# Performance work log

Hardware: AMD Instinct MI355X
Metric: run time of the kernel (lower is better)

The kernel has to match this reference:

```python
import jax, jax.numpy as jnp
import numpy as np

NUM_NODES = 20000
SEQ_LEN = 128
IN_FEATS = 2
HIDDEN = 32
N_TOTAL = NUM_NODES * SEQ_LEN  # flattened graph size
N_EDGES = 2_000_000


def setup_inputs() -> dict:
    key = jax.random.key(0)
    ks = jax.random.split(key, 10)
    x = jax.random.normal(ks[0], (NUM_NODES, SEQ_LEN, IN_FEATS), dtype=jnp.float32)
    edge_index = jax.random.randint(ks[1], (2, N_EDGES), 0, N_TOTAL, dtype=jnp.int64)
    s = 0.1
    gcn_W = jax.random.normal(ks[2], (IN_FEATS, HIDDEN), dtype=jnp.float32) * s
    gcn_b = jnp.zeros((HIDDEN,), dtype=jnp.float32)
    w_ih = jax.random.normal(ks[3], (4 * HIDDEN, HIDDEN), dtype=jnp.float32) * s
    w_hh = jax.random.normal(ks[4], (4 * HIDDEN, HIDDEN), dtype=jnp.float32) * s
    b_ih = jax.random.normal(ks[5], (4 * HIDDEN,), dtype=jnp.float32) * s
    b_hh = jax.random.normal(ks[6], (4 * HIDDEN,), dtype=jnp.float32) * s
    fc_W = jax.random.normal(ks[7], (HIDDEN, 1), dtype=jnp.float32) * s
    fc_b = jnp.zeros((1,), dtype=jnp.float32)
    return {"x": x, "edge_index": edge_index, "gcn_W": gcn_W, "gcn_b": gcn_b,
            "w_ih": w_ih, "w_hh": w_hh, "b_ih": b_ih, "b_hh": b_hh,
            "fc_W": fc_W, "fc_b": fc_b}


def _gcn(x_flat, edge_index, W, b):
    # PyG GCNConv: add self-loops, symmetric normalization, then linear+bias.
    src, dst = edge_index[0], edge_index[1]
    n = x_flat.shape[0]
    # degree at target side, including the self-loop (+1)
    deg = jax.ops.segment_sum(jnp.ones_like(dst, dtype=x_flat.dtype), dst, num_segments=n) + 1.0
    dinv = jax.lax.rsqrt(deg)  # deg >= 1 always (self-loop)
    h = x_flat @ W  # [n, HIDDEN] transform before propagate
    norm = dinv[src] * dinv[dst]  # [E]
    msg = h[src] * norm[:, None]  # gather + per-edge scale
    agg = jax.ops.segment_sum(msg, dst, num_segments=n)
    # self-loop contribution: dinv_i * dinv_i * h_i = h_i / deg_i
    out = agg + h * (1.0 / deg)[:, None]
    return out + b


def _lstm(xs, w_ih, w_hh, b_ih, b_hh):
    # torch LSTM gate order: i, f, g, o. xs: [N, S, H] -> final hidden [N, H]
    n, s, hdim = xs.shape
    xs_t = jnp.swapaxes(xs, 0, 1)  # [S, N, H]
    # precompute input projections once (dense GEMM)
    x_proj = xs_t @ w_ih.T + b_ih + b_hh  # [S, N, 4H]

    def step(carry, xp):
        h, c = carry
        g = xp + h @ w_hh.T  # [N, 4H]
        i, f, gg, o = jnp.split(g, 4, axis=-1)
        c = jax.nn.sigmoid(f) * c + jax.nn.sigmoid(i) * jnp.tanh(gg)
        h = jax.nn.sigmoid(o) * jnp.tanh(c)
        return (h, c), None

    h0 = jnp.zeros((n, hdim), dtype=xs.dtype)
    (hn, _), _ = jax.lax.scan(step, (h0, h0), x_proj)
    return hn


def reference(x, edge_index, gcn_W, gcn_b, w_ih, w_hh, b_ih, b_hh, fc_W, fc_b):
    num_nodes, seq_len, num_feats = x.shape
    x_in = x.reshape(-1, num_feats)  # [N*S, F]
    x_gcn = jax.nn.relu(_gcn(x_in, edge_index, gcn_W, gcn_b))
    x_lstm = x_gcn.reshape(num_nodes, seq_len, -1)
    hn = _lstm(x_lstm, w_ih, w_hh, b_ih, b_hh)
    return hn @ fc_W + fc_b  # [num_nodes, 1]
```

## Files before the change

kernel.cpp:

```cpp
#include <hip/hip_runtime.h>

#define SEQ 128
#define HID 32
#define TPB2 128
#define XS 40

typedef __attribute__((ext_vector_type(8))) short short8;
typedef __attribute__((ext_vector_type(4))) float floatx4;


__global__ void count_kernel(const int* __restrict__ idx, int E, int* __restrict__ cnt) {
    int e = (blockIdx.x * blockDim.x + threadIdx.x) * 4;
    if (((E & 3) == 0) && e + 3 < E) {
        int4 d = *(const int4*)(idx + E + e);
        atomicAdd(&cnt[d.x], 1);
        atomicAdd(&cnt[d.y], 1);
        atomicAdd(&cnt[d.z], 1);
        atomicAdd(&cnt[d.w], 1);
    } else {
        int lim = min(e + 4, E);
        for (int k = e; k < lim; ++k) atomicAdd(&cnt[idx[E + k]], 1);
    }
}

__device__ __forceinline__ unsigned long long pk2(float xx, float yy, float dv) {
    int qx = __float2int_rn(xx * dv * 2097152.0f);
    int qy = __float2int_rn(yy * dv * 2097152.0f);
    return ((unsigned long long)(unsigned)(qx + (1 << 26)) << 32) |
           (unsigned)(qy + (1 << 26));
}

__global__ void scatter_pk_kernel(const int* __restrict__ idx, int E,
                                  const float2* __restrict__ x2,
                                  const int* __restrict__ deg,
                                  unsigned long long* __restrict__ aggP) {
    int e = (blockIdx.x * blockDim.x + threadIdx.x) * 4;
    if (((E & 3) == 0) && e + 3 < E) {
        int4 s = *(const int4*)(idx + e);
        int4 d = *(const int4*)(idx + E + e);
        float2 v0 = x2[s.x];
        float2 v1 = x2[s.y];
        float2 v2 = x2[s.z];
        float2 v3 = x2[s.w];
        float dv0 = rsqrtf((float)deg[s.x] + 1.0f);
        float dv1 = rsqrtf((float)deg[s.y] + 1.0f);
        float dv2 = rsqrtf((float)deg[s.z] + 1.0f);
        float dv3 = rsqrtf((float)deg[s.w] + 1.0f);
        atomicAdd(&aggP[d.x], pk2(v0.x, v0.y, dv0));
        atomicAdd(&aggP[d.y], pk2(v1.x, v1.y, dv1));
        atomicAdd(&aggP[d.z], pk2(v2.x, v2.y, dv2));
        atomicAdd(&aggP[d.w], pk2(v3.x, v3.y, dv3));
    } else {
        int lim = min(e + 4, E);
        for (int k = e; k < lim; ++k) {
            int s = idx[k];
            int d = idx[E + k];
            float2 v = x2[s];
            float dv = rsqrtf((float)deg[s] + 1.0f);
            atomicAdd(&aggP[d], pk2(v.x, v.y, dv));
        }
    }
}


__device__ __forceinline__ float sg(float y) {
    return __builtin_amdgcn_rcpf(1.0f + __builtin_amdgcn_exp2f(-y));
}
__device__ __forceinline__ float tanh_f(float x) {
    return fmaf(__builtin_amdgcn_rcpf(1.0f + __expf(-2.0f * x)), 2.0f, -1.0f);
}
__device__ __forceinline__ void fsplit(float f, short& hi, short& lo) {
    unsigned u = __float_as_uint(f);
    hi = (short)(u >> 16);
    float r = f - __uint_as_float(u & 0xFFFF0000u);
    lo = (short)(__float_as_uint(r) >> 16);
}
__device__ __forceinline__ void fsplit2(float a, float b, unsigned& hi, unsigned& lo) {
    unsigned ta = __float_as_uint(a) & 0xFFFF0000u;
    unsigned tb = __float_as_uint(b) & 0xFFFF0000u;
    float ra = a - __uint_as_float(ta);
    float rb = b - __uint_as_float(tb);
    hi = __builtin_amdgcn_perm(__float_as_uint(b), __float_as_uint(a), 0x07060302u);
    lo = __builtin_amdgcn_perm(__float_as_uint(rb), __float_as_uint(ra), 0x07060302u);
}

__global__ __launch_bounds__(TPB2, 3) void lstm_sw3_kernel(
    const float2* __restrict__ x2,
    const unsigned long long* __restrict__ aggP, const int* __restrict__ deg,
    int N,
    const float* __restrict__ gcn_W, const float* __restrict__ gcn_b,
    const float* __restrict__ w_ih, const float* __restrict__ w_hh,
    const float* __restrict__ b_ih, const float* __restrict__ b_hh,
    const float* __restrict__ fc_W, const float* __restrict__ fc_b,
    float* __restrict__ out) {
    __shared__ float2 ubuf[16][SEQ + 1];
    __shared__ __align__(16) short hhb[2][16][XS];
    __shared__ __align__(16) short hlb[2][16][XS];
    __shared__ __align__(16) short xgh[2][16][XS];
    __shared__ __align__(16) short xgl[2][16][XS];
    __shared__ float fcp[2][16];

    const int tid = threadIdx.x;
    const int t1 = tid >> 6;
    const int lane = tid & 63;
    const int n = lane & 15;
    const int q = lane >> 4;
    const int base = blockIdx.x * 16;

    {
        const float2* xb = x2 + (size_t)base * SEQ;
        const unsigned long long* apb = aggP + (size_t)base * SEQ;
        const int* dgb = deg + (size_t)base * SEQ;
        const int lim = min(16 * SEQ, (N - base) * SEQ);
        for (int i = tid; i < 16 * SEQ; i += TPB2) {
            float2 v = make_float2(0.f, 0.f);
            if (i < lim) {
                int dg = dgb[i];
                float dv = rsqrtf((float)dg + 1.0f);
                float2 xx = xb[i];
                unsigned long long pk = apb[i];
                unsigned bias = (unsigned)dg * 67108864u;
                float ax = (float)((int)((unsigned)(pk >> 32) - bias)) * (1.0f / 2097152.0f);
                float ay = (float)((int)((unsigned)pk - bias)) * (1.0f / 2097152.0f);
                v = make_float2(dv * fmaf(xx.x, dv, ax), dv * fmaf(xx.y, dv, ay));
            }
            ubuf[i >> 7][i & 127] = v;
        }
        if (tid < 16) ubuf[tid][SEQ] = make_float2(0.f, 0.f);
        for (int i = tid; i < 320; i += TPB2) {
            ((int*)hhb[0])[i] = 0;
            ((int*)hlb[0])[i] = 0;
        }
    }

    short8 WiH[4], WiL[4], WhH[4], WhL[4];
    floatx4 biasv[4];
    #pragma unroll
    for (int g = 0; g < 4; ++g) {
        const float gsc = (g == 2) ? 2.8853900817779268f : 1.4426950408889634f;
        const int arow = g * 32 + 16 * t1 + n;
        const float* wi = w_ih + arow * HID + 8 * q;
        const float* wh = w_hh + arow * HID + 8 * q;
        #pragma unroll
        for (int j = 0; j < 8; ++j) {
            short h16, l16;
            fsplit(wi[j] * gsc, h16, l16); WiH[g][j] = h16; WiL[g][j] = l16;
            fsplit(wh[j] * gsc, h16, l16); WhH[g][j] = h16; WhL[g][j] = l16;
        }
        const float bb = (b_ih[arow] + b_hh[arow]) * gsc;
        biasv[g] = (floatx4){bb, bb, bb, bb};
    }

    float wgo0[4], wgo1[4], gbo[4];
    #pragma unroll
    for (int k = 0; k < 4; ++k) {
        const int uo = 16 * t1 + 4 * q + k;
        wgo0[k] = gcn_W[uo];
        wgo1[k] = gcn_W[HID + uo];
        gbo[k] = gcn_b[uo];
    }
    const float fcw = fc_W[16 * t1 + n];

    float c[4] = {0.f, 0.f, 0.f, 0.f};
    float ho[4] = {0.f, 0.f, 0.f, 0.f};

#define OWN_XG(PAR, TT)                                                           \
    {                                                                             \
        float2 uu = ubuf[n][TT];                                                  \
        float gv[4];                                                              \
        _Pragma("unroll") for (int k = 0; k < 4; ++k)                             \
            gv[k] = fmaxf(fmaf(uu.x, wgo0[k], fmaf(uu.y, wgo1[k], gbo[k])), 0.f); \
        unsigned hp0, lp0, hp1, lp1;                                              \
        fsplit2(gv[0], gv[1], hp0, lp0);                                          \
        fsplit2(gv[2], gv[3], hp1, lp1);                                          \
        uint2 th = make_uint2(hp0, hp1);                                          \
        uint2 tl = make_uint2(lp0, lp1);                                          \
        *(uint2*)&xgh[PAR][n][16 * t1 + 4 * q] = th;                              \
        *(uint2*)&xgl[PAR][n][16 * t1 + 4 * q] = tl;                              \
    }

    __syncthreads();
    OWN_XG(0, 0);
    __syncthreads();

#define LSTM_STEP(P, TT)                                                                    \
    do {                                                                                    \
        const short8 xh = *(const short8*)&xgh[P][n][8 * q];                                \
        const short8 xl = *(const short8*)&xgl[P][n][8 * q];                                \
        const short8 hh = *(const short8*)&hhb[P][n][8 * q];                                \
        const short8 hl = *(const short8*)&hlb[P][n][8 * q];                                \
        floatx4 acc[4];                                                                     \
        __builtin_amdgcn_s_setprio(1);                                                      \
        _Pragma("unroll") for (int g = 0; g < 4; ++g)                                       \
            acc[g] = __builtin_amdgcn_mfma_f32_16x16x32_bf16(xh, WiH[g], biasv[g], 0, 0, 0); \
        _Pragma("unroll") for (int g = 0; g < 4; ++g)                                       \
            acc[g] = __builtin_amdgcn_mfma_f32_16x16x32_bf16(xh, WiL[g], acc[g], 0, 0, 0);  \
        _Pragma("unroll") for (int g = 0; g < 4; ++g)                                       \
            acc[g] = __builtin_amdgcn_mfma_f32_16x16x32_bf16(xl, WiH[g], acc[g], 0, 0, 0);  \
        _Pragma("unroll") for (int g = 0; g < 4; ++g)                                       \
            acc[g] = __builtin_amdgcn_mfma_f32_16x16x32_bf16(hh, WhH[g], acc[g], 0, 0, 0);  \
        _Pragma("unroll") for (int g = 0; g < 4; ++g)                                       \
            acc[g] = __builtin_amdgcn_mfma_f32_16x16x32_bf16(hh, WhL[g], acc[g], 0, 0, 0);  \
        _Pragma("unroll") for (int g = 0; g < 4; ++g)                                       \
            acc[g] = __builtin_amdgcn_mfma_f32_16x16x32_bf16(hl, WhH[g], acc[g], 0, 0, 0);  \
        __builtin_amdgcn_s_setprio(0);                                                      \
        OWN_XG((P) ^ 1, (TT) + 1);         \
        _Pragma("unroll") for (int r = 0; r < 4; ++r) {                                     \
            const float ig = sg(acc[0][r]);                                                 \
            const float fg = sg(acc[1][r]);                                                 \
            const float gg = fmaf(sg(acc[2][r]), 2.0f, -1.0f);                              \
            const float og = sg(acc[3][r]);                                                 \
            c[r] = fmaf(fg, c[r], ig * gg);                                                 \
            const float hv = og * tanh_f(c[r]);                                             \
            ho[r] = hv;                                                                     \
            short h16, l16;                                                                 \
            fsplit(hv, h16, l16);                                                           \
            hhb[(P) ^ 1][4 * q + r][16 * t1 + n] = h16;                                     \
            hlb[(P) ^ 1][4 * q + r][16 * t1 + n] = l16;                                     \
        }                                                                                   \
        __syncthreads();                                                                    \
    } while (0)

    #pragma unroll 1
    for (int t = 0; t < SEQ; t += 2) {
        LSTM_STEP(0, t);
        LSTM_STEP(1, t + 1);
    }
#undef LSTM_STEP
#undef OWN_XG

    float p0 = ho[0] * fcw, p1 = ho[1] * fcw, p2 = ho[2] * fcw, p3 = ho[3] * fcw;
    #pragma unroll
    for (int m = 1; m < 16; m <<= 1) {
        p0 += __shfl_xor(p0, m);
        p1 += __shfl_xor(p1, m);
        p2 += __shfl_xor(p2, m);
        p3 += __shfl_xor(p3, m);
    }
    if (n == 0) {
        fcp[t1][4 * q + 0] = p0;
        fcp[t1][4 * q + 1] = p1;
        fcp[t1][4 * q + 2] = p2;
        fcp[t1][4 * q + 3] = p3;
    }
    __syncthreads();
    if (t1 == 0 && lane < 16) {
        const int node = base + lane;
        if (node < N) out[node] = fcp[0][lane] + fcp[1][lane] + fc_b[0];
    }
}

extern "C" void kernel_launch(void* const* d_in, const int* in_sizes, int n_in,
                              void* d_out, int out_size, void* d_ws, size_t ws_size,
                              hipStream_t stream) {
    const float* x     = (const float*)d_in[0];
    const int*   idx   = (const int*)d_in[1];
    const float* gcn_W = (const float*)d_in[2];
    const float* gcn_b = (const float*)d_in[3];
    const float* w_ih  = (const float*)d_in[4];
    const float* w_hh  = (const float*)d_in[5];
    const float* b_ih  = (const float*)d_in[6];
    const float* b_hh  = (const float*)d_in[7];
    const float* fc_W  = (const float*)d_in[8];
    const float* fc_b  = (const float*)d_in[9];

    const int num_nodes = in_sizes[0] / (SEQ * 2);
    const int ntot = num_nodes * SEQ;
    const int E = in_sizes[1] / 2;

    int* deg = (int*)d_ws;
    unsigned long long* aggP = (unsigned long long*)((char*)d_ws + (size_t)ntot * 4);

    hipMemsetAsync(d_ws, 0, (size_t)ntot * 12, stream);

    const int eb = (E + 1023) / 1024;
    count_kernel<<<eb, 256, 0, stream>>>(idx, E, deg);
    scatter_pk_kernel<<<eb, 256, 0, stream>>>(idx, E, (const float2*)x, deg, aggP);
    lstm_sw3_kernel<<<(num_nodes + 15) / 16, TPB2, 0, stream>>>(
        (const float2*)x, aggP, deg, num_nodes,
        gcn_W, gcn_b, w_ih, w_hh, b_ih, b_hh, fc_W, fc_b,
        (float*)d_out);
}
```

Measured before the change: 459.2 us.

## Process two independent 16-node groups per LSTM block to interleave MFMA chains

```diff
diff --git a/kernel.cpp b/kernel.cpp
--- a/kernel.cpp
+++ b/kernel.cpp
@@ -84,7 +84,7 @@
     lo = __builtin_amdgcn_perm(__float_as_uint(rb), __float_as_uint(ra), 0x07060302u);
 }
 
-__global__ __launch_bounds__(TPB2, 3) void lstm_sw3_kernel(
+__global__ __launch_bounds__(TPB2, 2) void lstm_sw4_kernel(
     const float2* __restrict__ x2,
     const unsigned long long* __restrict__ aggP, const int* __restrict__ deg,
     int N,
@@ -93,26 +93,26 @@
     const float* __restrict__ b_ih, const float* __restrict__ b_hh,
     const float* __restrict__ fc_W, const float* __restrict__ fc_b,
     float* __restrict__ out) {
-    __shared__ float2 ubuf[16][SEQ + 1];
-    __shared__ __align__(16) short hhb[2][16][XS];
-    __shared__ __align__(16) short hlb[2][16][XS];
-    __shared__ __align__(16) short xgh[2][16][XS];
-    __shared__ __align__(16) short xgl[2][16][XS];
-    __shared__ float fcp[2][16];
+    __shared__ float2 ubuf[32][SEQ + 1];
+    __shared__ __align__(16) short hhb[2][32][XS];
+    __shared__ __align__(16) short hlb[2][32][XS];
+    __shared__ __align__(16) short xgh[2][32][XS];
+    __shared__ __align__(16) short xgl[2][32][XS];
+    __shared__ float fcp[2][32];
 
     const int tid = threadIdx.x;
     const int t1 = tid >> 6;
     const int lane = tid & 63;
     const int n = lane & 15;
     const int q = lane >> 4;
-    const int base = blockIdx.x * 16;
+    const int base = blockIdx.x * 32;
 
     {
         const float2* xb = x2 + (size_t)base * SEQ;
         const unsigned long long* apb = aggP + (size_t)base * SEQ;
         const int* dgb = deg + (size_t)base * SEQ;
-        const int lim = min(16 * SEQ, (N - base) * SEQ);
-        for (int i = tid; i < 16 * SEQ; i += TPB2) {
+        const int lim = min(32 * SEQ, (N - base) * SEQ);
+        for (int i = tid; i < 32 * SEQ; i += TPB2) {
             float2 v = make_float2(0.f, 0.f);
             if (i < lim) {
                 int dg = dgb[i];
@@ -126,8 +126,8 @@
             }
             ubuf[i >> 7][i & 127] = v;
         }
-        if (tid < 16) ubuf[tid][SEQ] = make_float2(0.f, 0.f);
-        for (int i = tid; i < 320; i += TPB2) {
+        if (tid < 32) ubuf[tid][SEQ] = make_float2(0.f, 0.f);
+        for (int i = tid; i < 640; i += TPB2) {
             ((int*)hhb[0])[i] = 0;
             ((int*)hlb[0])[i] = 0;
         }
@@ -161,90 +161,133 @@
     }
     const float fcw = fc_W[16 * t1 + n];
 
-    float c[4] = {0.f, 0.f, 0.f, 0.f};
-    float ho[4] = {0.f, 0.f, 0.f, 0.f};
-
-#define OWN_XG(PAR, TT)                                                           \
+    float cA[4] = {0.f, 0.f, 0.f, 0.f}, hoA[4] = {0.f, 0.f, 0.f, 0.f};
+    float cB[4] = {0.f, 0.f, 0.f, 0.f}, hoB[4] = {0.f, 0.f, 0.f, 0.f};
+
+#define OWN_XG2(PAR, TT)                                                          \
     {                                                                             \
-        float2 uu = ubuf[n][TT];                                                  \
-        float gv[4];                                                              \
-        _Pragma("unroll") for (int k = 0; k < 4; ++k)                             \
-            gv[k] = fmaxf(fmaf(uu.x, wgo0[k], fmaf(uu.y, wgo1[k], gbo[k])), 0.f); \
-        unsigned hp0, lp0, hp1, lp1;                                              \
-        fsplit2(gv[0], gv[1], hp0, lp0);                                          \
-        fsplit2(gv[2], gv[3], hp1, lp1);                                          \
-        uint2 th = make_uint2(hp0, hp1);                                          \
-        uint2 tl = make_uint2(lp0, lp1);                                          \
-        *(uint2*)&xgh[PAR][n][16 * t1 + 4 * q] = th;                              \
-        *(uint2*)&xgl[PAR][n][16 * t1 + 4 * q] = tl;                              \
+        float2 ua = ubuf[n][TT];                                                  \
+        float2 ub = ubuf[16 + n][TT];                                             \
+        float ga[4], gb[4];                                                       \
+        _Pragma("unroll") for (int k = 0; k < 4; ++k) {                           \
+            ga[k] = fmaxf(fmaf(ua.x, wgo0[k], fmaf(ua.y, wgo1[k], gbo[k])), 0.f); \
+            gb[k] = fmaxf(fmaf(ub.x, wgo0[k], fmaf(ub.y, wgo1[k], gbo[k])), 0.f); \
+        }                                                                         \
+        unsigned h0, l0, h1, l1;                                                  \
+        fsplit2(ga[0], ga[1], h0, l0);                                            \
+        fsplit2(ga[2], ga[3], h1, l1);                                            \
+        *(uint2*)&xgh[PAR][n][16 * t1 + 4 * q] = make_uint2(h0, h1);              \
+        *(uint2*)&xgl[PAR][n][16 * t1 + 4 * q] = make_uint2(l0, l1);              \
+        fsplit2(gb[0], gb[1], h0, l0);                                            \
+        fsplit2(gb[2], gb[3], h1, l1);                                            \
+        *(uint2*)&xgh[PAR][16 + n][16 * t1 + 4 * q] = make_uint2(h0, h1);         \
+        *(uint2*)&xgl[PAR][16 + n][16 * t1 + 4 * q] = make_uint2(l0, l1);         \
     }
 
     __syncthreads();
-    OWN_XG(0, 0);
+    OWN_XG2(0, 0);
     __syncthreads();
 
-#define LSTM_STEP(P, TT)                                                                    \
-    do {                                                                                    \
-        const short8 xh = *(const short8*)&xgh[P][n][8 * q];                                \
-        const short8 xl = *(const short8*)&xgl[P][n][8 * q];                                \
-        const short8 hh = *(const short8*)&hhb[P][n][8 * q];                                \
-        const short8 hl = *(const short8*)&hlb[P][n][8 * q];                                \
-        floatx4 acc[4];                                                                     \
-        __builtin_amdgcn_s_setprio(1);                                                      \
-        _Pragma("unroll") for (int g = 0; g < 4; ++g)                                       \
-            acc[g] = __builtin_amdgcn_mfma_f32_16x16x32_bf16(xh, WiH[g], biasv[g], 0, 0, 0); \
-        _Pragma("unroll") for (int g = 0; g < 4; ++g)                                       \
-            acc[g] = __builtin_amdgcn_mfma_f32_16x16x32_bf16(xh, WiL[g], acc[g], 0, 0, 0);  \
-        _Pragma("unroll") for (int g = 0; g < 4; ++g)                                       \
-            acc[g] = __builtin_amdgcn_mfma_f32_16x16x32_bf16(xl, WiH[g], acc[g], 0, 0, 0);  \
-        _Pragma("unroll") for (int g = 0; g < 4; ++g)                                       \
-            acc[g] = __builtin_amdgcn_mfma_f32_16x16x32_bf16(hh, WhH[g], acc[g], 0, 0, 0);  \
-        _Pragma("unroll") for (int g = 0; g < 4; ++g)                                       \
-            acc[g] = __builtin_amdgcn_mfma_f32_16x16x32_bf16(hh, WhL[g], acc[g], 0, 0, 0);  \
-        _Pragma("unroll") for (int g = 0; g < 4; ++g)                                       \
-            acc[g] = __builtin_amdgcn_mfma_f32_16x16x32_bf16(hl, WhH[g], acc[g], 0, 0, 0);  \
-        __builtin_amdgcn_s_setprio(0);                                                      \
-        OWN_XG((P) ^ 1, (TT) + 1);         \
-        _Pragma("unroll") for (int r = 0; r < 4; ++r) {                                     \
-            const float ig = sg(acc[0][r]);                                                 \
-            const float fg = sg(acc[1][r]);                                                 \
-            const float gg = fmaf(sg(acc[2][r]), 2.0f, -1.0f);                              \
-            const float og = sg(acc[3][r]);                                                 \
-            c[r] = fmaf(fg, c[r], ig * gg);                                                 \
-            const float hv = og * tanh_f(c[r]);                                             \
-            ho[r] = hv;                                                                     \
-            short h16, l16;                                                                 \
-            fsplit(hv, h16, l16);                                                           \
-            hhb[(P) ^ 1][4 * q + r][16 * t1 + n] = h16;                                     \
-            hlb[(P) ^ 1][4 * q + r][16 * t1 + n] = l16;                                     \
-        }                                                                                   \
-        __syncthreads();                                                                    \
+#define LSTM_STEP2(P, TT)                                                                     \
+    do {                                                                                      \
+        const short8 xhA = *(const short8*)&xgh[P][n][8 * q];                                 \
+        const short8 xlA = *(const short8*)&xgl[P][n][8 * q];                                 \
+        const short8 hhA = *(const short8*)&hhb[P][n][8 * q];                                 \
+        const short8 hlA = *(const short8*)&hlb[P][n][8 * q];                                 \
+        const short8 xhB = *(const short8*)&xgh[P][16 + n][8 * q];                            \
+        const short8 xlB = *(const short8*)&xgl[P][16 + n][8 * q];                            \
+        const short8 hhB = *(const short8*)&hhb[P][16 + n][8 * q];                            \
+        const short8 hlB = *(const short8*)&hlb[P][16 + n][8 * q];                            \
+        floatx4 aA[4], aB[4];                                                                 \
+        __builtin_amdgcn_s_setprio(1);                                                        \
+        _Pragma("unroll") for (int g = 0; g < 4; ++g)                                         \
+            aA[g] = __builtin_amdgcn_mfma_f32_16x16x32_bf16(xhA, WiH[g], biasv[g], 0, 0, 0);  \
+        _Pragma("unroll") for (int g = 0; g < 4; ++g)                                         \
+            aB[g] = __builtin_amdgcn_mfma_f32_16x16x32_bf16(xhB, WiH[g], biasv[g], 0, 0, 0);  \
+        _Pragma("unroll") for (int g = 0; g < 4; ++g)                                         \
+            aA[g] = __builtin_amdgcn_mfma_f32_16x16x32_bf16(xhA, WiL[g], aA[g], 0, 0, 0);     \
+        _Pragma("unroll") for (int g = 0; g < 4; ++g)                                         \
+            aB[g] = __builtin_amdgcn_mfma_f32_16x16x32_bf16(xhB, WiL[g], aB[g], 0, 0, 0);     \
+        _Pragma("unroll") for (int g = 0; g < 4; ++g)                                         \
+            aA[g] = __builtin_amdgcn_mfma_f32_16x16x32_bf16(xlA, WiH[g], aA[g], 0, 0, 0);     \
+        _Pragma("unroll") for (int g = 0; g < 4; ++g)                                         \
+            aB[g] = __builtin_amdgcn_mfma_f32_16x16x32_bf16(xlB, WiH[g], aB[g], 0, 0, 0);     \
+        _Pragma("unroll") for (int g = 0; g < 4; ++g)                                         \
+            aA[g] = __builtin_amdgcn_mfma_f32_16x16x32_bf16(hhA, WhH[g], aA[g], 0, 0, 0);     \
+        _Pragma("unroll") for (int g = 0; g < 4; ++g)                                         \
+            aB[g] = __builtin_amdgcn_mfma_f32_16x16x32_bf16(hhB, WhH[g], aB[g], 0, 0, 0);     \
+        _Pragma("unroll") for (int g = 0; g < 4; ++g)                                         \
+            aA[g] = __builtin_amdgcn_mfma_f32_16x16x32_bf16(hhA, WhL[g], aA[g], 0, 0, 0);     \
+        _Pragma("unroll") for (int g = 0; g < 4; ++g)                                         \
+            aB[g] = __builtin_amdgcn_mfma_f32_16x16x32_bf16(hhB, WhL[g], aB[g], 0, 0, 0);     \
+        _Pragma("unroll") for (int g = 0; g < 4; ++g)                                         \
+            aA[g] = __builtin_amdgcn_mfma_f32_16x16x32_bf16(hlA, WhH[g], aA[g], 0, 0, 0);     \
+        _Pragma("unroll") for (int g = 0; g < 4; ++g)                                         \
+            aB[g] = __builtin_amdgcn_mfma_f32_16x16x32_bf16(hlB, WhH[g], aB[g], 0, 0, 0);     \
+        __builtin_amdgcn_s_setprio(0);                                                        \
+        OWN_XG2((P) ^ 1, (TT) + 1);           \
+        _Pragma("unroll") for (int r = 0; r < 4; ++r) {                                       \
+            const float ig = sg(aA[0][r]);                                                    \
+            const float fg = sg(aA[1][r]);                                                    \
+            const float gg = fmaf(sg(aA[2][r]), 2.0f, -1.0f);                                 \
+            const float og = sg(aA[3][r]);                                                    \
+            cA[r] = fmaf(fg, cA[r], ig * gg);                                                 \
+            const float hv = og * tanh_f(cA[r]);                                              \
+            hoA[r] = hv;                                                                      \
+            short h16, l16;                                                                   \
+            fsplit(hv, h16, l16);                                                             \
+            hhb[(P) ^ 1][4 * q + r][16 * t1 + n] = h16;                                       \
+            hlb[(P) ^ 1][4 * q + r][16 * t1 + n] = l16;                                       \
+        }                                                                                     \
+        _Pragma("unroll") for (int r = 0; r < 4; ++r) {                                       \
+            const float ig = sg(aB[0][r]);                                                    \
+            const float fg = sg(aB[1][r]);                                                    \
+            const float gg = fmaf(sg(aB[2][r]), 2.0f, -1.0f);                                 \
+            const float og = sg(aB[3][r]);                                                    \
+            cB[r] = fmaf(fg, cB[r], ig * gg);                                                 \
+            const float hv = og * tanh_f(cB[r]);                                              \
+            hoB[r] = hv;                                                                      \
+            short h16, l16;                                                                   \
+            fsplit(hv, h16, l16);                                                             \
+            hhb[(P) ^ 1][16 + 4 * q + r][16 * t1 + n] = h16;                                  \
+            hlb[(P) ^ 1][16 + 4 * q + r][16 * t1 + n] = l16;                                  \
+        }                                                                                     \
+        __syncthreads();                                                                      \
     } while (0)
 
     #pragma unroll 1
     for (int t = 0; t < SEQ; t += 2) {
-        LSTM_STEP(0, t);
-        LSTM_STEP(1, t + 1);
-    }
-#undef LSTM_STEP
-#undef OWN_XG
-
-    float p0 = ho[0] * fcw, p1 = ho[1] * fcw, p2 = ho[2] * fcw, p3 = ho[3] * fcw;
+        LSTM_STEP2(0, t);
+        LSTM_STEP2(1, t + 1);
+    }
+#undef LSTM_STEP2
+#undef OWN_XG2
+
+    float pA0 = hoA[0] * fcw, pA1 = hoA[1] * fcw, pA2 = hoA[2] * fcw, pA3 = hoA[3] * fcw;
+    float pB0 = hoB[0] * fcw, pB1 = hoB[1] * fcw, pB2 = hoB[2] * fcw, pB3 = hoB[3] * fcw;
     #pragma unroll
     for (int m = 1; m < 16; m <<= 1) {
-        p0 += __shfl_xor(p0, m);
-        p1 += __shfl_xor(p1, m);
-        p2 += __shfl_xor(p2, m);
-        p3 += __shfl_xor(p3, m);
+        pA0 += __shfl_xor(pA0, m);
+        pA1 += __shfl_xor(pA1, m);
+        pA2 += __shfl_xor(pA2, m);
+        pA3 += __shfl_xor(pA3, m);
+        pB0 += __shfl_xor(pB0, m);
+        pB1 += __shfl_xor(pB1, m);
+        pB2 += __shfl_xor(pB2, m);
+        pB3 += __shfl_xor(pB3, m);
     }
     if (n == 0) {
-        fcp[t1][4 * q + 0] = p0;
-        fcp[t1][4 * q + 1] = p1;
-        fcp[t1][4 * q + 2] = p2;
-        fcp[t1][4 * q + 3] = p3;
+        fcp[t1][4 * q + 0] = pA0;
+        fcp[t1][4 * q + 1] = pA1;
+        fcp[t1][4 * q + 2] = pA2;
+        fcp[t1][4 * q + 3] = pA3;
+        fcp[t1][16 + 4 * q + 0] = pB0;
+        fcp[t1][16 + 4 * q + 1] = pB1;
+        fcp[t1][16 + 4 * q + 2] = pB2;
+        fcp[t1][16 + 4 * q + 3] = pB3;
     }
     __syncthreads();
-    if (t1 == 0 && lane < 16) {
+    if (t1 == 0 && lane < 32) {
         const int node = base + lane;
         if (node < N) out[node] = fcp[0][lane] + fcp[1][lane] + fc_b[0];
     }
@@ -276,7 +319,7 @@
     const int eb = (E + 1023) / 1024;
     count_kernel<<<eb, 256, 0, stream>>>(idx, E, deg);
     scatter_pk_kernel<<<eb, 256, 0, stream>>>(idx, E, (const float2*)x, deg, aggP);
-    lstm_sw3_kernel<<<(num_nodes + 15) / 16, TPB2, 0, stream>>>(
+    lstm_sw4_kernel<<<(num_nodes + 31) / 32, TPB2, 0, stream>>>(
         (const float2*)x, aggP, deg, num_nodes,
         gcn_W, gcn_b, w_ih, w_hh, b_ih, b_hh, fc_W, fc_b,
         (float*)d_out);
```

Measured after the change: 524.6 us. +14.2%, slower.
